# Optimization experiments

Hardware: AMD Instinct MI355X
Metric: run time of the kernel (lower is better)

The kernel has to match this reference:

```python
import jax, jax.numpy as jnp
import numpy as np

BATCH = 4096
CTX = 20
HASH = 1_000_000        # word_hash_size / num_classes
DIM = 128               # word_embedding_size
NUM_SAMPLED = 8192
NEG_INF = -1e9          # accidental-hit masking (TF subtracts a huge constant)


def _log_expected_count(ids):
    # TF LogUniformCandidateSampler: P(c) = (log(c+2) - log(c+1)) / log(range_max + 1)
    # expected_count(c) = -expm1(num_sampled * log1p(-P(c)))  (sampling w/o replacement approx)
    ids_f = ids.astype(jnp.float32)
    p = (jnp.log(ids_f + 2.0) - jnp.log(ids_f + 1.0)) / jnp.log(jnp.float32(HASH + 1))
    return jnp.log(-jnp.expm1(jnp.float32(NUM_SAMPLED) * jnp.log1p(-p)))


def setup_inputs() -> dict:
    key = jax.random.key(0)
    k1, k2, k3, k4, k5, k6 = jax.random.split(key, 6)
    return {
        "input_ids": jax.random.randint(k1, (BATCH, CTX), 0, HASH, dtype=jnp.int64)
        if jax.config.jax_enable_x64 else jax.random.randint(k1, (BATCH, CTX), 0, HASH).astype(jnp.int32),
        "labels": jax.random.randint(k2, (BATCH,), 0, HASH).astype(jnp.int32),
        "sampled_ids": jax.random.randint(k3, (NUM_SAMPLED,), 0, HASH).astype(jnp.int32),
        "input_emb": jax.random.normal(k4, (HASH, DIM), dtype=jnp.float32) * 0.05,
        "output_emb": jax.random.normal(k5, (HASH, DIM), dtype=jnp.float32) * 0.05,
        "output_bias": jax.random.normal(k6, (HASH,), dtype=jnp.float32) * 0.05,
    }


def reference(input_ids, labels, sampled_ids, input_emb, output_emb, output_bias):
    # --- input-side: gather + sum-pool over context window -> [B, D]
    h = jnp.sum(input_emb[input_ids], axis=1)

    # --- sampled softmax (training path of the model) ---
    # true logits: per-example dot with the true class row  -> [B]
    w_true = output_emb[labels]                      # [B, D]
    true_logits = jnp.einsum("bd,bd->b", h, w_true) + output_bias[labels]
    true_logits = true_logits - _log_expected_count(labels)

    # sampled logits: shared negative set -> [B, S]
    w_samp = output_emb[sampled_ids]                 # [S, D]
    sampled_logits = jnp.einsum("bd,sd->bs", h, w_samp) + output_bias[sampled_ids][None, :]
    sampled_logits = sampled_logits - _log_expected_count(sampled_ids)[None, :]

    # remove accidental hits (sampled id == true label)
    hit = sampled_ids[None, :] == labels[:, None]    # [B, S]
    sampled_logits = jnp.where(hit, jnp.float32(NEG_INF), sampled_logits)

    # softmax cross entropy with the true class at column 0
    logits = jnp.concatenate([true_logits[:, None], sampled_logits], axis=1)  # [B, 1+S]
    loss = jax.nn.logsumexp(logits, axis=1) - true_logits                      # [B]
    return loss
```

## Files before the change

### kernel.cpp

```cpp
#include <hip/hip_runtime.h>
#include <hip/hip_bf16.h>
#include <math.h>

#define BATCH 4096
#define CTX 20
#define DIM 128
#define NSAMP 8192
#define NCHUNK 64

typedef __attribute__((ext_vector_type(8))) short short8;
typedef __attribute__((ext_vector_type(4))) float f32x4;

__device__ __forceinline__ unsigned short f2bf(float x) {
    union { float f; unsigned u; } v; v.f = x;
    unsigned r = v.u + 0x7FFFu + ((v.u >> 16) & 1u);
    return (unsigned short)(r >> 16);
}

__device__ __forceinline__ float eigen_plogf(float xf) {
    union { float f; unsigned u; } v; v.f = xf;
    int ei = (int)((v.u >> 23) & 0xFFu) - 126;
    v.u = (v.u & 0x007FFFFFu) | 0x3F000000u;
    float x = v.f;
    float e = (float)ei;
    bool msk = x < 0.707106781186547524f;
    float tmp = msk ? x : 0.0f;
    x = __fsub_rn(x, 1.0f);
    e = __fsub_rn(e, msk ? 1.0f : 0.0f);
    x = __fadd_rn(x, tmp);

    float x2 = __fmul_rn(x, x);
    float x3 = __fmul_rn(x2, x);

    float y, y1, y2;
    y  = __builtin_fmaf( 7.0376836292E-2f, x, -1.1514610310E-1f);
    y1 = __builtin_fmaf(-1.2420140846E-1f, x,  1.4249322787E-1f);
    y2 = __builtin_fmaf( 2.0000714765E-1f, x, -2.4999993993E-1f);
    y  = __builtin_fmaf(y,  x,  1.1676998740E-1f);
    y1 = __builtin_fmaf(y1, x, -1.6668057665E-1f);
    y2 = __builtin_fmaf(y2, x,  3.3333331174E-1f);
    y  = __builtin_fmaf(y,  x3, y1);
    y  = __builtin_fmaf(y,  x3, y2);
    y  = __fmul_rn(y, x3);

    y1  = __fmul_rn(e, -2.12194440e-4f);
    tmp = __fmul_rn(x2, 0.5f);
    y   = __fadd_rn(y, y1);
    x   = __fsub_rn(x, tmp);
    y2  = __fmul_rn(e, 0.693359375f);
    x   = __fadd_rn(x, y);
    x   = __fadd_rn(x, y2);
    return x;
}

__device__ __forceinline__ float log_expected_count(int id) {
    float idf = (float)id;
    float l2 = eigen_plogf(__fadd_rn(idf, 2.0f));
    float l1 = eigen_plogf(__fadd_rn(idf, 1.0f));
    float num = __fsub_rn(l2, l1);
    float logH = eigen_plogf(1000001.0f);
    float p = num / logH;
    float t = __fmul_rn(8192.0f, log1pf(-p));
    float e = -expm1f(t);
    e = fmaxf(e, 1e-38f);
    return logf(e);
}

__device__ __forceinline__ size_t frag_off(int row, int k0) {
    return (size_t)(((row >> 4) * 4 + (k0 >> 5)) * 512) +
           ((((k0 >> 3) & 3) * 16 + (row & 15)) * 8) + (k0 & 7);
}

__global__ __launch_bounds__(256) void k_prep(
        const int* __restrict__ ids, const int* __restrict__ labels,
        const int* __restrict__ sampled,
        const float* __restrict__ in_emb, const float* __restrict__ out_emb,
        const float* __restrict__ bias,
        unsigned short* __restrict__ h_frag, unsigned short* __restrict__ w_frag,
        float* __restrict__ tl, float* __restrict__ sb) {
    int tid  = threadIdx.x;
    int lane = tid & 63;
    int wv   = tid >> 6;
    int task = blockIdx.x * 4 + wv;
    int half = lane >> 5;
    int m    = lane & 31;
    int k0   = 4 * m;

    if (task < BATCH) {
        int b = task;
        float4 s4 = make_float4(0.f, 0.f, 0.f, 0.f);
#pragma unroll
        for (int c = 0; c < CTX; c += 2) {
            int id = ids[b * CTX + c + half];
            float4 v = *(const float4*)(in_emb + (size_t)id * DIM + k0);
            s4.x += v.x; s4.y += v.y; s4.z += v.z; s4.w += v.w;
        }
        s4.x += __shfl_xor(s4.x, 32, 64);
        s4.y += __shfl_xor(s4.y, 32, 64);
        s4.z += __shfl_xor(s4.z, 32, 64);
        s4.w += __shfl_xor(s4.w, 32, 64);

        if (half == 0) {
            ushort4 hb;
            hb.x = f2bf(s4.x); hb.y = f2bf(s4.y); hb.z = f2bf(s4.z); hb.w = f2bf(s4.w);
            *(ushort4*)(h_frag + frag_off(b, k0)) = hb;
        }
        int lab = labels[b];
        float4 w4 = *(const float4*)(out_emb + (size_t)lab * DIM + k0);
        float prod = s4.x * w4.x + s4.y * w4.y + s4.z * w4.z + s4.w * w4.w;
#pragma unroll
        for (int mm = 16; mm > 0; mm >>= 1) prod += __shfl_xor(prod, mm, 64);
        if (lane == 0) tl[b] = prod + bias[lab] - log_expected_count(lab);
    } else {
        int s = (task - BATCH) * 2 + half;
        int sid = sampled[s];
        float4 v = *(const float4*)(out_emb + (size_t)sid * DIM + k0);
        ushort4 wb;
        wb.x = f2bf(v.x); wb.y = f2bf(v.y); wb.z = f2bf(v.z); wb.w = f2bf(v.w);
        *(ushort4*)(w_frag + frag_off(s, k0)) = wb;
        if (m == 0) sb[s] = bias[sid] - log_expected_count(sid);
    }
}

__global__ __launch_bounds__(256, 3) void k_gemm_lse(
    const unsigned short* __restrict__ h_frag, const unsigned short* __restrict__ w_frag,
    const float* __restrict__ sb, const int* __restrict__ sampled,
    const int* __restrict__ labels, float* __restrict__ partials) {
    __shared__ __align__(16) unsigned short ldsb[16384];
    int tid  = threadIdx.x;
    int lane = tid & 63;
    int wv   = tid >> 6;
    int r16  = lane & 15;
    int kg   = lane >> 4;
    int rbase = blockIdx.x * 128 + wv * 32;
    int cbase = blockIdx.y * 128;

    const unsigned short* wsrc = w_frag + (size_t)cbase * 128;
#pragma unroll
    for (int i = 0; i < 8; ++i) {
        int eo = (i * 256 + tid) * 8;
        __builtin_amdgcn_global_load_lds(
            (const __attribute__((address_space(1))) unsigned int*)(wsrc + eo),
            (__attribute__((address_space(3))) unsigned int*)(ldsb + eo),
            16, 0, 0);
    }

    short8 a[2][4];
#pragma unroll
    for (int rt = 0; rt < 2; ++rt)
#pragma unroll
        for (int ks = 0; ks < 4; ++ks)
            a[rt][ks] = *(const short8*)(h_frag +
                (size_t)((((rbase >> 4) + rt) * 4 + ks) * 512) + lane * 8);

    f32x4 acc[2][8];
#pragma unroll
    for (int rt = 0; rt < 2; ++rt)
#pragma unroll
        for (int t = 0; t < 8; ++t) acc[rt][t] = (f32x4){0.f, 0.f, 0.f, 0.f};

    __syncthreads();
#pragma unroll
    for (int t = 0; t < 8; ++t) {
#pragma unroll
        for (int ks = 0; ks < 4; ++ks) {
            short8 bv = *(const short8*)(ldsb + (t * 4 + ks) * 512 + lane * 8);
#pragma unroll
            for (int rt = 0; rt < 2; ++rt)
                acc[rt][t] = __builtin_amdgcn_mfma_f32_16x16x32_bf16(a[rt][ks], bv, acc[rt][t], 0, 0, 0);
        }
    }

    int lab[2][4];
    float rsum[2][4];
#pragma unroll
    for (int rt = 0; rt < 2; ++rt)
#pragma unroll
        for (int r = 0; r < 4; ++r) {
            lab[rt][r]  = labels[rbase + rt * 16 + kg * 4 + r];
            rsum[rt][r] = 0.f;
        }
#pragma unroll
    for (int t = 0; t < 8; ++t) {
        int col = cbase + t * 16 + r16;
        float sbv = sb[col];
        int   sid = sampled[col];
#pragma unroll
        for (int rt = 0; rt < 2; ++rt)
#pragma unroll
            for (int r = 0; r < 4; ++r) {
                float logit = acc[rt][t][r] + sbv;
                if (sid != lab[rt][r]) rsum[rt][r] += __expf(logit);
            }
    }
#pragma unroll
    for (int m = 1; m < 16; m <<= 1)
#pragma unroll
        for (int rt = 0; rt < 2; ++rt)
#pragma unroll
            for (int r = 0; r < 4; ++r)
                rsum[rt][r] += __shfl_xor(rsum[rt][r], m, 64);
    if (r16 == 0)
#pragma unroll
        for (int rt = 0; rt < 2; ++rt)
#pragma unroll
            for (int r = 0; r < 4; ++r)
                partials[(size_t)(rbase + rt * 16 + kg * 4 + r) * NCHUNK + blockIdx.y] = rsum[rt][r];
}

__global__ void k_reduce(const float* __restrict__ partials, const float* __restrict__ tl,
                         float* __restrict__ out) {
    int row  = blockIdx.x * 4 + (threadIdx.x >> 6);
    int lane = threadIdx.x & 63;
    float s = partials[(size_t)row * NCHUNK + lane];
#pragma unroll
    for (int m = 32; m > 0; m >>= 1) s += __shfl_xor(s, m, 64);
    if (lane == 0) {
        float t = tl[row];
        out[row] = logf(s + __expf(t)) - t;
    }
}

extern "C" void kernel_launch(void* const* d_in, const int* in_sizes, int n_in,
                              void* d_out, int out_size, void* d_ws, size_t ws_size,
                              hipStream_t stream) {
    const int*   ids     = (const int*)d_in[0];
    const int*   labels  = (const int*)d_in[1];
    const int*   sampled = (const int*)d_in[2];
    const float* in_emb  = (const float*)d_in[3];
    const float* out_emb = (const float*)d_in[4];
    const float* bias    = (const float*)d_in[5];
    float* out = (float*)d_out;

    char* ws = (char*)d_ws;
    unsigned short* h_frag = (unsigned short*)(ws);
    unsigned short* w_frag = (unsigned short*)(ws + (1u << 20));
    float* tl       = (float*)(ws + 3u * (1u << 20));
    float* sb       = (float*)(ws + 3u * (1u << 20) + (1u << 16));
    float* partials = (float*)(ws + 3u * (1u << 20) + (1u << 16) + (1u << 15));

    k_prep<<<dim3((BATCH + NSAMP / 2) / 4), dim3(256), 0, stream>>>(
        ids, labels, sampled, in_emb, out_emb, bias, h_frag, w_frag, tl, sb);
    k_gemm_lse<<<dim3(BATCH / 128, NSAMP / 128), dim3(256), 0, stream>>>(
        h_frag, w_frag, sb, sampled, labels, partials);
    k_reduce<<<dim3(BATCH / 4), dim3(256), 0, stream>>>(partials, tl, out);
}
```

Measured before the change: 34.47 us.

## Move accidental-hit masking out of GEMM epilogue via hash table correction

The GEMM epilogue no longer compares sampled ids against labels. It now sums exp over all columns, using exp2 with the bias and log-expected-count term pre-scaled by log2(e). Accidental hits are subtracted afterwards in the reduce kernel: each label is looked up in a hash table of sampled ids built with atomicCAS during prep, and the matching logits are recomputed from the bf16 fragments. This removes per-element compares and label/sampled loads from the hot epilogue, but adds a memset, atomics and probing. The subtraction can also lose precision when the hit term dominates the row sum.

```diff
diff --git a/kernel.cpp b/kernel.cpp
--- a/kernel.cpp
+++ b/kernel.cpp
@@ -7,6 +7,8 @@
 #define DIM 128
 #define NSAMP 8192
 #define NCHUNK 64
+#define HSLOTS 16384
+#define LOG2E 1.44269504088896340736f
 
 typedef __attribute__((ext_vector_type(8))) short short8;
 typedef __attribute__((ext_vector_type(4))) float f32x4;
@@ -15,6 +17,9 @@
     union { float f; unsigned u; } v; v.f = x;
     unsigned r = v.u + 0x7FFFu + ((v.u >> 16) & 1u);
     return (unsigned short)(r >> 16);
+}
+__device__ __forceinline__ float bf2f(unsigned short u) {
+    union { float f; unsigned v; } w; w.v = ((unsigned)u) << 16; return w.f;
 }
 
 __device__ __forceinline__ float eigen_plogf(float xf) {
@@ -77,7 +82,8 @@
         const float* __restrict__ in_emb, const float* __restrict__ out_emb,
         const float* __restrict__ bias,
         unsigned short* __restrict__ h_frag, unsigned short* __restrict__ w_frag,
-        float* __restrict__ tl, float* __restrict__ sb) {
+        float* __restrict__ tl, float* __restrict__ sb2,
+        unsigned long long* __restrict__ htab) {
     int tid  = threadIdx.x;
     int lane = tid & 63;
     int wv   = tid >> 6;
@@ -118,14 +124,19 @@
         ushort4 wb;
         wb.x = f2bf(v.x); wb.y = f2bf(v.y); wb.z = f2bf(v.z); wb.w = f2bf(v.w);
         *(ushort4*)(w_frag + frag_off(s, k0)) = wb;
-        if (m == 0) sb[s] = bias[sid] - log_expected_count(sid);
+        if (m == 0) {
+            sb2[s] = (bias[sid] - log_expected_count(sid)) * LOG2E;
+            unsigned long long packed = (((unsigned long long)sid) << 13) | (unsigned)s;
+            unsigned p = ((unsigned)sid * 2654435761u) & (HSLOTS - 1);
+            while (atomicCAS(&htab[p], ~0ULL, packed) != ~0ULL)
+                p = (p + 1) & (HSLOTS - 1);
+        }
     }
 }
 
 __global__ __launch_bounds__(256, 3) void k_gemm_lse(
     const unsigned short* __restrict__ h_frag, const unsigned short* __restrict__ w_frag,
-    const float* __restrict__ sb, const int* __restrict__ sampled,
-    const int* __restrict__ labels, float* __restrict__ partials) {
+    const float* __restrict__ sb2, float* __restrict__ partials) {
     __shared__ __align__(16) unsigned short ldsb[16384];
     int tid  = threadIdx.x;
     int lane = tid & 63;
@@ -171,27 +182,16 @@
         }
     }
 
-    int lab[2][4];
-    float rsum[2][4];
-#pragma unroll
-    for (int rt = 0; rt < 2; ++rt)
-#pragma unroll
-        for (int r = 0; r < 4; ++r) {
-            lab[rt][r]  = labels[rbase + rt * 16 + kg * 4 + r];
-            rsum[rt][r] = 0.f;
-        }
+    float rsum[2][4] = {{0.f,0.f,0.f,0.f},{0.f,0.f,0.f,0.f}};
 #pragma unroll
     for (int t = 0; t < 8; ++t) {
         int col = cbase + t * 16 + r16;
-        float sbv = sb[col];
-        int   sid = sampled[col];
+        float s2 = sb2[col];
 #pragma unroll
         for (int rt = 0; rt < 2; ++rt)
 #pragma unroll
-            for (int r = 0; r < 4; ++r) {
-                float logit = acc[rt][t][r] + sbv;
-                if (sid != lab[rt][r]) rsum[rt][r] += __expf(logit);
-            }
+            for (int r = 0; r < 4; ++r)
+                rsum[rt][r] += exp2f(__builtin_fmaf(acc[rt][t][r], LOG2E, s2));
     }
 #pragma unroll
     for (int m = 1; m < 16; m <<= 1)
@@ -209,12 +209,38 @@
 }
 
 __global__ void k_reduce(const float* __restrict__ partials, const float* __restrict__ tl,
+                         const int* __restrict__ labels, const float* __restrict__ sb2,
+                         const unsigned short* __restrict__ h_frag,
+                         const unsigned short* __restrict__ w_frag,
+                         const unsigned long long* __restrict__ htab,
                          float* __restrict__ out) {
     int row  = blockIdx.x * 4 + (threadIdx.x >> 6);
     int lane = threadIdx.x & 63;
     float s = partials[(size_t)row * NCHUNK + lane];
 #pragma unroll
     for (int m = 32; m > 0; m >>= 1) s += __shfl_xor(s, m, 64);
+
+    int lab = labels[row];
+    unsigned p = ((unsigned)lab * 2654435761u) & (HSLOTS - 1);
+    float h0 = 0.f, h1 = 0.f;
+    {
+        ushort2 hv = *(const ushort2*)(h_frag + frag_off(row, 2 * lane));
+        h0 = bf2f(hv.x); h1 = bf2f(hv.y);
+    }
+    while (true) {
+        unsigned long long slot = htab[p];
+        if (slot == ~0ULL) break;
+        if ((int)(slot >> 13) == lab) {
+            int sc = (int)(slot & 8191u);
+            ushort2 wv = *(const ushort2*)(w_frag + frag_off(sc, 2 * lane));
+            float d = h0 * bf2f(wv.x) + h1 * bf2f(wv.y);
+#pragma unroll
+            for (int m = 32; m > 0; m >>= 1) d += __shfl_xor(d, m, 64);
+            s -= exp2f(__builtin_fmaf(d, LOG2E, sb2[sc]));
+        }
+        p = (p + 1) & (HSLOTS - 1);
+    }
+
     if (lane == 0) {
         float t = tl[row];
         out[row] = logf(s + __expf(t)) - t;
@@ -236,12 +262,16 @@
     unsigned short* h_frag = (unsigned short*)(ws);
     unsigned short* w_frag = (unsigned short*)(ws + (1u << 20));
     float* tl       = (float*)(ws + 3u * (1u << 20));
-    float* sb       = (float*)(ws + 3u * (1u << 20) + (1u << 16));
+    float* sb2      = (float*)(ws + 3u * (1u << 20) + (1u << 16));
     float* partials = (float*)(ws + 3u * (1u << 20) + (1u << 16) + (1u << 15));
+    unsigned long long* htab = (unsigned long long*)(ws + 5u * (1u << 20));
+
+    hipMemsetAsync(htab, 0xFF, HSLOTS * sizeof(unsigned long long), stream);
 
     k_prep<<<dim3((BATCH + NSAMP / 2) / 4), dim3(256), 0, stream>>>(
-        ids, labels, sampled, in_emb, out_emb, bias, h_frag, w_frag, tl, sb);
+        ids, labels, sampled, in_emb, out_emb, bias, h_frag, w_frag, tl, sb2, htab);
     k_gemm_lse<<<dim3(BATCH / 128, NSAMP / 128), dim3(256), 0, stream>>>(
-        h_frag, w_frag, sb, sampled, labels, partials);
-    k_reduce<<<dim3(BATCH / 4), dim3(256), 0, stream>>>(partials, tl, out);
-}
+        h_frag, w_frag, sb2, partials);
+    k_reduce<<<dim3(BATCH / 4), dim3(256), 0, stream>>>(
+        partials, tl, labels, sb2, h_frag, w_frag, htab, out);
+}
```

Result: slower. 50.95 us (+47.8%).
